# Optimization experiments

Measured on AMD Instinct MI355X. Metric: run time of the kernel, lower is better.

The kernel has to match this reference:

```python
import jax, jax.numpy as jnp
import numpy as np

KA = 2  # kernel_att == stride

def _unfold2(t):
    # torch nn.Unfold(kernel=2, stride=2, pad=0): [B,C,H,W] -> [B, C, 4, L], L=(H/2)*(W/2)
    B, C, H, W = t.shape
    t = t.reshape(B, C, H // KA, KA, W // KA, KA).transpose(0, 1, 3, 5, 2, 4)
    return t.reshape(B, C, KA * KA, (H // KA) * (W // KA))

def _fold2(t, H, W):
    # inverse of _unfold2 (non-overlapping): [B, C, 4, L] -> [B, C, H, W]
    B, C, _, L = t.shape
    t = t.reshape(B, C, KA, KA, H // KA, W // KA).transpose(0, 1, 4, 2, 5, 3)
    return t.reshape(B, C, H, W)

def setup_inputs() -> dict:
    key = jax.random.key(0)
    ks = jax.random.split(key, 5)
    b, c, m, h, w = 4, 16, 8, 64, 64
    O = 64
    return {
        "x": jax.random.normal(ks[0], (b, c, m, h, w), jnp.float32),
        "w_q": jax.random.normal(ks[1], (O, m), jnp.float32) * 0.1,
        "w_k": jax.random.normal(ks[2], (O, m), jnp.float32) * 0.1,
        "w_v": jax.random.normal(ks[3], (O, m), jnp.float32) * 0.1,
        "w_p": jax.random.normal(ks[4], (2,), jnp.float32) * 0.1,
    }

def reference(x, w_q, w_k, w_v, w_p):
    b, c, m, h, w = x.shape
    O = w_q.shape[0]
    # res = AdaptiveAvgPool3d((1, dim, dim)) with h==w==dim -> mean over m only
    res = x.mean(axis=2, keepdims=True)            # [b, c, 1, h, w]
    xf = x.reshape(b * c, m, h, w)
    # 1x1 convs (bias-free) are channel matmuls
    q = jnp.einsum('om,bmhw->bohw', w_q, xf)       # [b*c, O, h, w]
    k = jnp.einsum('om,bmhw->bohw', w_k, xf)
    v = jnp.einsum('om,bmhw->bohw', w_v, xf)
    # relative position map pe = conv_p(position(h, w)) -> [1,1,h,w]
    loc_w = jnp.linspace(-1.0, 1.0, w)[None, :]    # varies along W
    loc_h = jnp.linspace(-1.0, 1.0, h)[:, None]    # varies along H
    pe = (w_p[0] * loc_w + w_p[1] * loc_h)[None, None]  # [1,1,h,w]
    q5 = q.reshape(b, c, O, h, w).transpose(0, 2, 1, 3, 4)  # permuted: [b, O, c, h, w]
    k5 = k.reshape(b, c, O, h, w) + pe             # pe broadcast over trailing (h,w)
    v5 = v.reshape(b, c, O, h, w)
    scaling = float(h) ** (-0.5)
    B = b * O
    q_att = (q5 * scaling).reshape(B, c, h, w)
    # NB: torch code views the UNpermuted [b,c,O,h,w] buffer as [b*O, c, h, w] (raw reinterpretation)
    k_att = k5.reshape(B, c, h, w)
    v_att = v5.reshape(B, c, h, w)
    uq = _unfold2(q_att)                           # [B, c, 4, L]
    uk = _unfold2(k_att) + _unfold2(pe)            # unfold_rpe broadcast: [B, c, 4, L]
    uv = _unfold2(v_att)
    # att[B,i,j,l] = sum_p q[B,i,p,l] * k[B,j,p,l]
    att = jnp.einsum('bipl,bjpl->bijl', uq, uk)    # [B, c, c, L]
    att = jax.nn.softmax(att, axis=2)
    out = jnp.einsum('bijl,bjpl->bipl', att, uv)   # [B, c, 4, L]
    out = _fold2(out, h, w)                        # [B, c, h, w]
    out = out.reshape(b, O, c, h, w).transpose(0, 2, 1, 3, 4)  # [b, c, O, h, w]
    return out + res
```

## Files before the change

kernel.cpp:

```cpp
#include <hip/hip_runtime.h>

typedef float v2f __attribute__((ext_vector_type(2)));


__global__ __launch_bounds__(256, 6) void adapt_attn(
    const float* __restrict__ x,  const float* __restrict__ wq,
    const float* __restrict__ wk, const float* __restrict__ wv,
    const float* __restrict__ wp, float* __restrict__ out)
{
    __shared__ __align__(16) float s_wk[128];
    __shared__ __align__(16) float s_wv[128];
    __shared__ float  s_wq[8];
    __shared__ v2f    s_xk[8][2][16];
    __shared__ float4 s_uk[16][16];
    __shared__ float4 s_uv[16][16];

    const int tid = threadIdx.x;
    const int bid = blockIdx.x;
    const int tile = bid & 63;
    const int o    = (bid >> 6) & 63;
    const int bb   = bid >> 12;
    const int r = o & 3, qch = o >> 2;
    const int y0  = (tile >> 1) << 1;
    const int ww0 = (tile & 1) << 4;

    if (tid < 128) {
        s_wk[tid] = wk[(r << 7) + tid];
        s_wv[tid] = wv[(r << 7) + tid];
    } else if (tid < 136) {
        s_wq[tid - 128] = 0.125f * wq[(o << 3) + (tid - 128)];
    }

    const v2f* __restrict__ x2 = (const v2f*)x;

    {
        const int p = tid & 15, row = (tid >> 4) & 1, m = tid >> 5;
        const int g = ((bb << 4) + qch) * 16384 + m * 2048 + (y0 + row) * 32 + ww0 + p;
        s_xk[m][row][p] = x2[g];
    }
    __syncthreads();

    {
        const int p = tid & 15, j = tid >> 4;
        const float wp0 = wp[0], wp1 = wp[1];
        const float step = 2.0f / 63.0f;
        const int wwp = ww0 + p;
        const float lx0 = -1.0f + step * (float)(wwp << 1);
        const float lx1 = lx0 + step;
        const float ly0 = -1.0f + step * (float)y0;
        const float ly1 = ly0 + step;
        v2f ka = { 2.0f * (wp0 * lx0 + wp1 * ly0), 2.0f * (wp0 * lx1 + wp1 * ly0) };
        v2f kb = { 2.0f * (wp0 * lx0 + wp1 * ly1), 2.0f * (wp0 * lx1 + wp1 * ly1) };
        v2f va = {0.f, 0.f}, vb = {0.f, 0.f};

        float wkj[8], wvj[8];
        *(float4*)&wkj[0] = ((const float4*)s_wk)[j * 2];
        *(float4*)&wkj[4] = ((const float4*)s_wk)[j * 2 + 1];
        *(float4*)&wvj[0] = ((const float4*)s_wv)[j * 2];
        *(float4*)&wvj[4] = ((const float4*)s_wv)[j * 2 + 1];

        #pragma unroll
        for (int m = 0; m < 8; m++) {
            const v2f xa = s_xk[m][0][p];
            const v2f xb = s_xk[m][1][p];
            ka += xa * wkj[m]; kb += xb * wkj[m];
            va += xa * wvj[m]; vb += xb * wvj[m];
        }
        s_uk[j][p] = make_float4(ka.x, ka.y, kb.x, kb.y);
        s_uv[j][p] = make_float4(va.x, va.y, vb.x, vb.y);
    }
    __syncthreads();

    {
        const int p = tid & 15, i = tid >> 4;
        float wqr[8];
        #pragma unroll
        for (int m = 0; m < 8; m++) wqr[m] = s_wq[m];

        const int bq = ((bb << 4) + i) * 16384 + y0 * 32 + ww0 + p;
        v2f qa[8], qb[8];
        #pragma unroll
        for (int m = 0; m < 8; m++) {
            qa[m] = x2[bq + m * 2048];
            qb[m] = x2[bq + m * 2048 + 32];
        }
        v2f uqa = {0.f,0.f}, uqb = {0.f,0.f}, rsa = {0.f,0.f}, rsb = {0.f,0.f};
        #pragma unroll
        for (int m = 0; m < 8; m++) {
            uqa += qa[m] * wqr[m];
            uqb += qb[m] * wqr[m];
            rsa += qa[m];
            rsb += qb[m];
        }

        float att[16];
        float sum = 0.f;
        #pragma unroll
        for (int j = 0; j < 16; j++) {
            const float4 k4 = s_uk[j][p];
            v2f t = uqa * (v2f){k4.x, k4.y};
            t += uqb * (v2f){k4.z, k4.w};
            const float e = __expf(t.x + t.y);
            att[j] = e;
            sum += e;
        }
        const float rcp = 1.0f / sum;

        v2f oa = {0.f,0.f}, ob = {0.f,0.f};
        #pragma unroll
        for (int j = 0; j < 16; j++) {
            const float4 v4 = s_uv[j][p];
            oa += (v2f){v4.x, v4.y} * att[j];
            ob += (v2f){v4.z, v4.w} * att[j];
        }
        oa = oa * rcp + rsa * 0.125f;
        ob = ob * rcp + rsb * 0.125f;

        v2f* __restrict__ out2 = (v2f*)out;
        const int obi = (((bb << 4) + i) * 64 + o) * 2048 + y0 * 32 + ww0 + p;
        out2[obi]      = oa;
        out2[obi + 32] = ob;
    }
}

extern "C" void kernel_launch(void* const* d_in, const int* in_sizes, int n_in,
                              void* d_out, int out_size, void* d_ws, size_t ws_size,
                              hipStream_t stream) {
    const float* x  = (const float*)d_in[0];
    const float* wq = (const float*)d_in[1];
    const float* wk = (const float*)d_in[2];
    const float* wv = (const float*)d_in[3];
    const float* wp = (const float*)d_in[4];
    float* out = (float*)d_out;
    adapt_attn<<<dim3(16384), dim3(256), 0, stream>>>(x, wq, wk, wv, wp, out);
}
```

Before: 125.0 us.

## Process two spatial tiles per block and two query channels per thread

Each block now handles two adjacent spatial tiles, which halves the grid and amortizes the weight loads into shared memory and the barriers over more work. In the attention stage each thread computes two query rows and reuses every k/v value it reads from shared memory for both. The softmax and the weighted V sum are fused into a single pass, so the att[16] array is no longer kept. The cost is higher register pressure (launch bounds lowered to 4 blocks) and fewer blocks to hide latency.

```diff
diff --git a/kernel.cpp b/kernel.cpp
--- a/kernel.cpp
+++ b/kernel.cpp
@@ -3,7 +3,7 @@
 typedef float v2f __attribute__((ext_vector_type(2)));
 
 
-__global__ __launch_bounds__(256, 6) void adapt_attn(
+__global__ __launch_bounds__(256, 4) void adapt_attn(
     const float* __restrict__ x,  const float* __restrict__ wq,
     const float* __restrict__ wk, const float* __restrict__ wv,
     const float* __restrict__ wp, float* __restrict__ out)
@@ -11,18 +11,16 @@
     __shared__ __align__(16) float s_wk[128];
     __shared__ __align__(16) float s_wv[128];
     __shared__ float  s_wq[8];
-    __shared__ v2f    s_xk[8][2][16];
-    __shared__ float4 s_uk[16][16];
-    __shared__ float4 s_uv[16][16];
+    __shared__ v2f    s_xk[2][8][2][16];
+    __shared__ float4 s_uk[2][16][16];
+    __shared__ float4 s_uv[2][16][16];
 
     const int tid = threadIdx.x;
     const int bid = blockIdx.x;
-    const int tile = bid & 63;
-    const int o    = (bid >> 6) & 63;
-    const int bb   = bid >> 12;
+    const int tg = bid & 31;
+    const int o  = (bid >> 5) & 63;
+    const int bb = bid >> 11;
     const int r = o & 3, qch = o >> 2;
-    const int y0  = (tile >> 1) << 1;
-    const int ww0 = (tile & 1) << 4;
 
     if (tid < 128) {
         s_wk[tid] = wk[(r << 7) + tid];
@@ -33,17 +31,25 @@
 
     const v2f* __restrict__ x2 = (const v2f*)x;
 
-    {
-        const int p = tid & 15, row = (tid >> 4) & 1, m = tid >> 5;
-        const int g = ((bb << 4) + qch) * 16384 + m * 2048 + (y0 + row) * 32 + ww0 + p;
-        s_xk[m][row][p] = x2[g];
+    #pragma unroll
+    for (int it = 0; it < 2; it++) {
+        const int idx = it * 256 + tid;
+        const int p = idx & 15, row = (idx >> 4) & 1, m = (idx >> 5) & 7, t = idx >> 8;
+        const int tile = tg * 2 + t;
+        const int y0 = (tile >> 1) << 1, ww0 = (tile & 1) << 4;
+        s_xk[t][m][row][p] =
+            x2[((bb * 16 + qch) * 8 + m) * 2048 + (y0 + row) * 32 + ww0 + p];
     }
     __syncthreads();
 
-    {
-        const int p = tid & 15, j = tid >> 4;
-        const float wp0 = wp[0], wp1 = wp[1];
-        const float step = 2.0f / 63.0f;
+    const float wp0 = wp[0], wp1 = wp[1];
+    const float step = 2.0f / 63.0f;
+    #pragma unroll
+    for (int it = 0; it < 2; it++) {
+        const int idx = it * 256 + tid;
+        const int p = idx & 15, j = (idx >> 4) & 15, t = idx >> 8;
+        const int tile = tg * 2 + t;
+        const int y0 = (tile >> 1) << 1, ww0 = (tile & 1) << 4;
         const int wwp = ww0 + p;
         const float lx0 = -1.0f + step * (float)(wwp << 1);
         const float lx1 = lx0 + step;
@@ -61,65 +67,93 @@
 
         #pragma unroll
         for (int m = 0; m < 8; m++) {
-            const v2f xa = s_xk[m][0][p];
-            const v2f xb = s_xk[m][1][p];
+            const v2f xa = s_xk[t][m][0][p];
+            const v2f xb = s_xk[t][m][1][p];
             ka += xa * wkj[m]; kb += xb * wkj[m];
             va += xa * wvj[m]; vb += xb * wvj[m];
         }
-        s_uk[j][p] = make_float4(ka.x, ka.y, kb.x, kb.y);
-        s_uv[j][p] = make_float4(va.x, va.y, vb.x, vb.y);
+        s_uk[t][j][p] = make_float4(ka.x, ka.y, kb.x, kb.y);
+        s_uv[t][j][p] = make_float4(va.x, va.y, vb.x, vb.y);
     }
     __syncthreads();
 
     {
-        const int p = tid & 15, i = tid >> 4;
+        const int p = tid & 15, ig = (tid >> 4) & 7, t = tid >> 7;
+        const int tile = tg * 2 + t;
+        const int y0 = (tile >> 1) << 1, ww0 = (tile & 1) << 4;
+        const int sp = y0 * 32 + ww0 + p;
+
         float wqr[8];
         #pragma unroll
         for (int m = 0; m < 8; m++) wqr[m] = s_wq[m];
 
-        const int bq = ((bb << 4) + i) * 16384 + y0 * 32 + ww0 + p;
-        v2f qa[8], qb[8];
+        v2f uqa[2], uqb[2], rsa[2], rsb[2];
         #pragma unroll
-        for (int m = 0; m < 8; m++) {
-            qa[m] = x2[bq + m * 2048];
-            qb[m] = x2[bq + m * 2048 + 32];
-        }
-        v2f uqa = {0.f,0.f}, uqb = {0.f,0.f}, rsa = {0.f,0.f}, rsb = {0.f,0.f};
-        #pragma unroll
-        for (int m = 0; m < 8; m++) {
-            uqa += qa[m] * wqr[m];
-            uqb += qb[m] * wqr[m];
-            rsa += qa[m];
-            rsb += qb[m];
+        for (int n = 0; n < 2; n++) {
+            const int i = ig * 2 + n;
+            const int bq = (bb * 16 + i) * 16384 + sp;
+            v2f qa[8], qb[8];
+            #pragma unroll
+            for (int m = 0; m < 8; m++) {
+                qa[m] = x2[bq + m * 2048];
+                qb[m] = x2[bq + m * 2048 + 32];
+            }
+            v2f ua = {0.f, 0.f}, ub = {0.f, 0.f}, ra = {0.f, 0.f}, rb = {0.f, 0.f};
+            #pragma unroll
+            for (int m = 0; m < 8; m++) {
+                ua += qa[m] * wqr[m];
+                ub += qb[m] * wqr[m];
+                ra += qa[m];
+                rb += qb[m];
+            }
+            uqa[n] = ua; uqb[n] = ub; rsa[n] = ra; rsb[n] = rb;
         }
 
-        float att[16];
-        float sum = 0.f;
+        v2f oa0 = {0.f, 0.f}, ob0 = {0.f, 0.f};
+        v2f oa1 = {0.f, 0.f}, ob1 = {0.f, 0.f};
+        float sum0 = 0.f, sum1 = 0.f;
+
         #pragma unroll
         for (int j = 0; j < 16; j++) {
-            const float4 k4 = s_uk[j][p];
-            v2f t = uqa * (v2f){k4.x, k4.y};
-            t += uqb * (v2f){k4.z, k4.w};
-            const float e = __expf(t.x + t.y);
-            att[j] = e;
-            sum += e;
+            const float4 k4 = s_uk[t][j][p];
+            const float4 v4 = s_uv[t][j][p];
+            const v2f ka = {k4.x, k4.y}, kb = {k4.z, k4.w};
+            const v2f va = {v4.x, v4.y}, vb = {v4.z, v4.w};
+
+            v2f t0 = uqa[0] * ka;
+            t0 += uqb[0] * kb;
+            const float e0 = __expf(t0.x + t0.y);
+            sum0 += e0;
+            oa0 += va * e0;
+            ob0 += vb * e0;
+
+            v2f t1 = uqa[1] * ka;
+            t1 += uqb[1] * kb;
+            const float e1 = __expf(t1.x + t1.y);
+            sum1 += e1;
+            oa1 += va * e1;
+            ob1 += vb * e1;
         }
-        const float rcp = 1.0f / sum;
-
-        v2f oa = {0.f,0.f}, ob = {0.f,0.f};
-        #pragma unroll
-        for (int j = 0; j < 16; j++) {
-            const float4 v4 = s_uv[j][p];
-            oa += (v2f){v4.x, v4.y} * att[j];
-            ob += (v2f){v4.z, v4.w} * att[j];
-        }
-        oa = oa * rcp + rsa * 0.125f;
-        ob = ob * rcp + rsb * 0.125f;
 
         v2f* __restrict__ out2 = (v2f*)out;
-        const int obi = (((bb << 4) + i) * 64 + o) * 2048 + y0 * 32 + ww0 + p;
-        out2[obi]      = oa;
-        out2[obi + 32] = ob;
+        {
+            const int i = ig * 2;
+            const float rcp = 1.0f / sum0;
+            const v2f outa = oa0 * rcp + rsa[0] * 0.125f;
+            const v2f outb = ob0 * rcp + rsb[0] * 0.125f;
+            const int obi = ((bb * 16 + i) * 64 + o) * 2048 + sp;
+            out2[obi]      = outa;
+            out2[obi + 32] = outb;
+        }
+        {
+            const int i = ig * 2 + 1;
+            const float rcp = 1.0f / sum1;
+            const v2f outa = oa1 * rcp + rsa[1] * 0.125f;
+            const v2f outb = ob1 * rcp + rsb[1] * 0.125f;
+            const int obi = ((bb * 16 + i) * 64 + o) * 2048 + sp;
+            out2[obi]      = outa;
+            out2[obi + 32] = outb;
+        }
     }
 }
 
@@ -132,5 +166,5 @@
     const float* wv = (const float*)d_in[3];
     const float* wp = (const float*)d_in[4];
     float* out = (float*)d_out;
-    adapt_attn<<<dim3(16384), dim3(256), 0, stream>>>(x, wq, wk, wv, wp, out);
+    adapt_attn<<<dim3(8192), dim3(256), 0, stream>>>(x, wq, wk, wv, wp, out);
 }
```

New measurement: 121.0 us. -3.3%, faster.
